# Kernel optimization log

Hardware: AMD Instinct MI355X
Metric: run time of the kernel (lower is better)

Reference implementation:

```python
import jax, jax.numpy as jnp
import numpy as np

NUM_HEADS = 16

def setup_inputs() -> dict:
    key = jax.random.key(0)
    k1, k2, k3 = jax.random.split(key, 3)
    B, T, C = 4, 2048, 2048
    x = jax.random.normal(k1, (B, T, C), dtype=jnp.float32)
    Wqkv = jax.random.normal(k2, (C, 3 * C), dtype=jnp.float32) * (C ** -0.5)
    bqkv = jnp.zeros((3 * C,), dtype=jnp.float32)
    Wproj = jax.random.normal(k3, (C, C), dtype=jnp.float32) * (C ** -0.5)
    bproj = jnp.zeros((C,), dtype=jnp.float32)
    return {"x": x, "Wqkv": Wqkv, "bqkv": bqkv, "Wproj": Wproj, "bproj": bproj}

def reference(x, Wqkv, bqkv, Wproj, bproj):
    B, T, C = x.shape
    H = NUM_HEADS
    D = C // H  # head_dim
    qkv = x @ Wqkv + bqkv                      # [B,T,3C]
    q, k, v = jnp.split(qkv, 3, axis=-1)
    # [B,T,C] -> [B,H,T,D]
    q = q.reshape(B, T, H, D).transpose(0, 2, 1, 3)
    k = k.reshape(B, T, H, D).transpose(0, 2, 1, 3)
    v = v.reshape(B, T, H, D).transpose(0, 2, 1, 3)
    scale = D ** -0.5
    scores = jnp.einsum('bhqd,bhkd->bhqk', q, k) * scale  # [B,H,T,T]
    causal = jnp.tril(jnp.ones((T, T), dtype=bool))
    scores = jnp.where(causal, scores, jnp.finfo(scores.dtype).min)
    attn = jax.nn.softmax(scores, axis=-1)
    out = jnp.einsum('bhqk,bhkd->bhqd', attn, v)           # [B,H,T,D]
    out = out.transpose(0, 2, 1, 3).reshape(B, T, C)
    return out @ Wproj + bproj
```

## Files before the change

kernel.cpp:

```cpp
#include <hip/hip_runtime.h>
#include <hip/hip_bf16.h>
#include <stdint.h>

typedef __attribute__((ext_vector_type(8))) short short8;
typedef __attribute__((ext_vector_type(4))) float f32x4;
typedef __attribute__((ext_vector_type(16))) float f32x16;
typedef __attribute__((ext_vector_type(2))) unsigned int uint2v;

__device__ __forceinline__ unsigned short f2bf(float f) {
  union { float f; unsigned int u; } v; v.f = f;
  unsigned int r = v.u + 0x7FFFu + ((v.u >> 16) & 1u);
  return (unsigned short)(r >> 16);
}

__device__ __forceinline__ unsigned int cvtpk(float lo, float hi) {
  unsigned int r;
  asm("v_cvt_pk_bf16_f32 %0, %1, %2" : "=v"(r) : "v"(lo), "v"(hi));
  return r;
}

#define GLOAD16(gsrc, ldst)                                                                  \
  __builtin_amdgcn_global_load_lds((const __attribute__((address_space(1))) void*)(gsrc),    \
                                   (__attribute__((address_space(3))) void*)(ldst), 16, 0, 0)

#define BAR() __builtin_amdgcn_s_barrier()
#define LGKMC(n) do { asm volatile("s_waitcnt lgkmcnt(" #n ")" ::: "memory"); \
                      __builtin_amdgcn_sched_barrier(0); } while (0)
#define LGKM0() LGKMC(0)
#define VMCNT0() asm volatile("s_waitcnt vmcnt(0)" ::: "memory")
#define VMCNT8() do { asm volatile("s_waitcnt vmcnt(8)" ::: "memory"); \
                      __builtin_amdgcn_sched_barrier(0); } while (0)
#define PRIO(x) __builtin_amdgcn_s_setprio(x)
#define MFMA16(d, a, b) d = __builtin_amdgcn_mfma_f32_16x16x32_bf16(a, b, d, 0, 0, 0)

__global__ __launch_bounds__(256) void preproc_kernel(const float* __restrict__ x,
                                                      const float* __restrict__ Wqkv,
                                                      const float* __restrict__ Wproj,
                                                      unsigned short* __restrict__ x_bf,
                                                      unsigned short* __restrict__ wqkvt,
                                                      unsigned short* __restrict__ wprojt) {
  __shared__ float tile[32][33];
  int blk = blockIdx.x;
  int tid = threadIdx.x;
  if (blk < 16384) {
    int i = blk * 256 + tid;
    float4 v = ((const float4*)x)[i];
    ushort4 o;
    o.x = f2bf(v.x); o.y = f2bf(v.y); o.z = f2bf(v.z); o.w = f2bf(v.w);
    ((ushort4*)x_bf)[i] = o;
    return;
  }
  const float* W;
  unsigned short* Wt;
  int n0, k0, N;
  if (blk < 16384 + 12288) {
    int b = blk - 16384;
    W = Wqkv; Wt = wqkvt; N = 6144;
    n0 = (b % 192) * 32; k0 = (b / 192) * 32;
  } else {
    int b = blk - 16384 - 12288;
    W = Wproj; Wt = wprojt; N = 2048;
    n0 = (b & 63) * 32; k0 = (b >> 6) * 32;
  }
  int tx = tid & 31, ty = tid >> 5;
#pragma unroll
  for (int j = 0; j < 32; j += 8)
    tile[ty + j][tx] = W[(size_t)(k0 + ty + j) * N + n0 + tx];
  __syncthreads();
#pragma unroll
  for (int j = 0; j < 32; j += 8)
    Wt[(size_t)(n0 + ty + j) * 2048 + k0 + tx] = f2bf(tile[tx][ty + j]);
}

__device__ __forceinline__ void stageA128(const unsigned short* __restrict__ gp, int K,
                                          int kt, char* lds, int tid) {
#pragma unroll
  for (int it = 0; it < 4; ++it) {
    int li = it * 256 + tid;
    int r = li >> 3, c = li & 7;
    GLOAD16(gp + (size_t)r * K + kt * 64 + (c ^ (r & 7)) * 8, lds + li * 16);
  }
}
__device__ __forceinline__ void stageB256(const unsigned short* __restrict__ gp, int K,
                                          int kt, char* lds, int tid) {
#pragma unroll
  for (int it = 0; it < 8; ++it) {
    int li = it * 256 + tid;
    int r = li >> 3, c = li & 7;
    GLOAD16(gp + (size_t)r * K + kt * 64 + (c ^ (r & 7)) * 8, lds + li * 16);
  }
}

__device__ __forceinline__ void gemm128x256_mainloop(const unsigned short* __restrict__ Ap,
                                                     const unsigned short* __restrict__ Bp,
                                                     int K, int tid, char* smem,
                                                     f32x4 acc[4][8]) {
  char* sa = smem;
  char* sb = smem + 16384;
  const int KT = K >> 6;

  int wid = tid >> 6, lane = tid & 63;
  int wr = wid >> 1, wc = wid & 1;
  int lg = lane >> 4, l15 = lane & 15;
  int swz7 = l15 & 7;

#define LDA(m, kc) \
  (*(const short8*)((const unsigned short*)sa + (size_t)((wr * 64 + (m) * 16 + l15) * 64 + ((((kc) * 4 + lg) ^ swz7) * 8))))
#define LDB(n, kc) \
  (*(const short8*)((const unsigned short*)sb + (size_t)((wc * 128 + (n) * 16 + l15) * 64 + ((((kc) * 4 + lg) ^ swz7) * 8))))

  stageA128(Ap, K, 0, sa, tid);
  stageB256(Bp, K, 0, sb, tid);
  VMCNT0();
  BAR();

  for (int t = 0; t < KT; ++t) {
    short8 aq[4][2], bq[4][2];
#pragma unroll
    for (int m = 0; m < 4; ++m) { aq[m][0] = LDA(m, 0); aq[m][1] = LDA(m, 1); }
#pragma unroll
    for (int n = 0; n < 4; ++n) { bq[n][0] = LDB(n, 0); bq[n][1] = LDB(n, 1); }
    LGKM0();
    PRIO(1);
#pragma unroll
    for (int kc = 0; kc < 2; ++kc)
#pragma unroll
      for (int m = 0; m < 4; ++m)
#pragma unroll
        for (int n = 0; n < 4; ++n)
          MFMA16(acc[m][n], aq[m][kc], bq[n][kc]);
    PRIO(0);
#pragma unroll
    for (int n = 0; n < 4; ++n) { bq[n][0] = LDB(n + 4, 0); bq[n][1] = LDB(n + 4, 1); }
    LGKM0();
    PRIO(1);
#pragma unroll
    for (int kc = 0; kc < 2; ++kc)
#pragma unroll
      for (int m = 0; m < 4; ++m)
#pragma unroll
        for (int n = 0; n < 4; ++n)
          MFMA16(acc[m][n + 4], aq[m][kc], bq[n][kc]);
    PRIO(0);
    BAR();
    if (t + 1 < KT) {
      stageA128(Ap, K, t + 1, sa, tid);
      stageB256(Bp, K, t + 1, sb, tid);
      VMCNT0();
    }
    BAR();
  }
#undef LDA
#undef LDB
}

__device__ __forceinline__ void stage_half(const unsigned short* __restrict__ gp, int K,
                                           int kt, int half, char* lds_mat, int tid) {
#pragma unroll
  for (int it = 0; it < 2; ++it) {
    int li = half * 1024 + it * 512 + tid;
    int r = li >> 3, c = li & 7;
    int cs = c ^ (r & 7);
    GLOAD16(gp + (size_t)r * K + kt * 64 + cs * 8, lds_mat + li * 16);
  }
}

__device__ __forceinline__ void gemm256sq_mainloop(const unsigned short* __restrict__ Ap,
                                                   const unsigned short* __restrict__ Bp,
                                                   int K, int tid, char* smem,
                                                   f32x4 acc[8][4]) {
  char* sa = smem;
  char* sb = smem + 65536;
  const int KT = K >> 6;

  int wid = tid >> 6, lane = tid & 63;
  int wr = wid >> 2, wc = wid & 3;
  int lg = lane >> 4, l15 = lane & 15;
  int swz7 = l15 & 7;

#define LDA2(ab, m, kc) \
  (*(const short8*)((const unsigned short*)(ab) + (size_t)((wr * 128 + (m) * 16 + l15) * 64 + ((((kc) * 4 + lg) ^ swz7) * 8))))
#define LDB2(bb, n, kc) \
  (*(const short8*)((const unsigned short*)(bb) + (size_t)((wc * 64 + (n) * 16 + l15) * 64 + ((((kc) * 4 + lg) ^ swz7) * 8))))

  stage_half(Bp, K, 0, 0, sb, tid);
  stage_half(Bp, K, 0, 1, sb, tid);
  stage_half(Ap, K, 0, 0, sa, tid);
  stage_half(Ap, K, 0, 1, sa, tid);
  stage_half(Bp, K, 1, 0, sb + 32768, tid);
  stage_half(Bp, K, 1, 1, sb + 32768, tid);
  stage_half(Ap, K, 1, 0, sa + 32768, tid);
  stage_half(Ap, K, 1, 1, sa + 32768, tid);
  VMCNT8();
  BAR();

  for (int t = 0; t < KT; ++t) {
    int p = t & 1;
    const char* ab = sa + p * 32768;
    const char* bb = sb + p * 32768;
    int kt2 = (t + 2 < KT) ? t + 2 : KT - 1;

    short8 bq01[2][2], bq23[2][2], aq[4][2], aq2[4][2];
#pragma unroll
    for (int n = 0; n < 2; ++n) { bq01[n][0] = LDB2(bb, n, 0); bq01[n][1] = LDB2(bb, n, 1); }
#pragma unroll
    for (int m = 0; m < 4; ++m) { aq[m][0] = LDA2(ab, m, 0); aq[m][1] = LDA2(ab, m, 1); }
#pragma unroll
    for (int n = 0; n < 2; ++n) { bq23[n][0] = LDB2(bb, n + 2, 0); bq23[n][1] = LDB2(bb, n + 2, 1); }
#pragma unroll
    for (int m = 0; m < 4; ++m) { aq2[m][0] = LDA2(ab, m + 4, 0); aq2[m][1] = LDA2(ab, m + 4, 1); }

    LGKMC(12);
    PRIO(1);
#pragma unroll
    for (int kc = 0; kc < 2; ++kc)
#pragma unroll
      for (int m = 0; m < 4; ++m)
#pragma unroll
        for (int n = 0; n < 2; ++n)
          MFMA16(acc[m][n], aq[m][kc], bq01[n][kc]);
    PRIO(0);

    LGKMC(8);
    BAR();
    stage_half(Bp, K, kt2, 0, sb + p * 32768, tid);
    stage_half(Bp, K, kt2, 1, sb + p * 32768, tid);

    PRIO(1);
#pragma unroll
    for (int kc = 0; kc < 2; ++kc)
#pragma unroll
      for (int m = 0; m < 4; ++m)
#pragma unroll
        for (int n = 0; n < 2; ++n)
          MFMA16(acc[m][n + 2], aq[m][kc], bq23[n][kc]);
    PRIO(0);

    LGKMC(0);
    PRIO(1);
#pragma unroll
    for (int kc = 0; kc < 2; ++kc)
#pragma unroll
      for (int m = 0; m < 4; ++m)
#pragma unroll
        for (int n = 0; n < 2; ++n)
          MFMA16(acc[m + 4][n + 2], aq2[m][kc], bq23[n][kc]);
    PRIO(0);

    BAR();
    stage_half(Ap, K, kt2, 0, sa + p * 32768, tid);
    stage_half(Ap, K, kt2, 1, sa + p * 32768, tid);
    PRIO(1);
#pragma unroll
    for (int kc = 0; kc < 2; ++kc)
#pragma unroll
      for (int m = 0; m < 4; ++m)
#pragma unroll
        for (int n = 0; n < 2; ++n)
          MFMA16(acc[m + 4][n], aq2[m][kc], bq01[n][kc]);
    PRIO(0);
    VMCNT8();
    BAR();
  }
#undef LDA2
#undef LDB2
}

__global__ __launch_bounds__(256, 2) void gemm_qkv256_kernel(const unsigned short* __restrict__ A,
                                                             const unsigned short* __restrict__ Bt,
                                                             const float* __restrict__ bias,
                                                             unsigned short* __restrict__ qb,
                                                             unsigned short* __restrict__ kb,
                                                             unsigned short* __restrict__ vtb) {
  extern __shared__ char smem[];
  int wg = blockIdx.x;
  int xcd = wg & 7, idx = wg >> 3;
  int bn = xcd * 3 + idx % 3;
  int bm = idx / 3;
  int tid = threadIdx.x;

  f32x4 acc[4][8];
  f32x4 zero = {0.f, 0.f, 0.f, 0.f};
#pragma unroll
  for (int m = 0; m < 4; ++m)
#pragma unroll
    for (int n = 0; n < 8; ++n) acc[m][n] = zero;

  gemm128x256_mainloop(A + (size_t)bm * 128 * 2048, Bt + (size_t)bn * 256 * 2048, 2048, tid, smem, acc);

  const float QSCALE = (float)(0.08838834764831845 * 1.4426950408889634);
  int wid = tid >> 6, lane = tid & 63;
  int wr = wid >> 1, wc = wid & 1, lg = lane >> 4, l15 = lane & 15;

  if (bn >= 16) {
    int h0v = (bn - 16) * 2;
#pragma unroll
    for (int n = 0; n < 8; ++n) {
      int cl = wc * 128 + n * 16 + l15;
      float bv = bias[bn * 256 + cl];
#pragma unroll
      for (int m = 0; m < 4; ++m) {
        int rl = wr * 64 + m * 16 + lg * 4;
        unsigned int w0 = cvtpk(acc[m][n][0] + bv, acc[m][n][1] + bv);
        unsigned int w1 = cvtpk(acc[m][n][2] + bv, acc[m][n][3] + bv);
        uint2v pk = {w0, w1};
        *(uint2v*)(smem + cl * 256 + ((rl * 2) ^ ((cl & 7) << 4))) = pk;
      }
    }
    LGKM0();
    BAR();
    int b = (bm * 128) >> 11, t0 = (bm * 128) & 2047;
#pragma unroll
    for (int i = 0; i < 16; ++i) {
      int id = i * 256 + tid;
      int dloc = id >> 4, c = id & 15;
      short8 v = *(const short8*)(smem + dloc * 256 + ((c * 16) ^ ((dloc & 7) << 4)));
      int bh_ = b * 16 + h0v + (dloc >> 7);
      int d = dloc & 127;
      *(short8*)(vtb + ((size_t)bh_ * 128 + d) * 2048 + t0 + c * 8) = v;
    }
  } else {
    bool isq = (bn < 8);
#pragma unroll
    for (int n = 0; n < 8; ++n) {
      int cl = wc * 128 + n * 16 + l15;
      float bv = bias[bn * 256 + cl];
#pragma unroll
      for (int m = 0; m < 4; ++m) {
#pragma unroll
        for (int g = 0; g < 4; ++g) {
          int rl = wr * 64 + m * 16 + lg * 4 + g;
          float r = acc[m][n][g] + bv;
          if (isq) r *= QSCALE;
          *(unsigned short*)(smem + rl * 512 + ((cl * 2) ^ ((rl & 15) << 4))) = f2bf(r);
        }
      }
    }
    LGKM0();
    BAR();
    unsigned short* dst = isq ? qb : kb;
    int h0 = (bn & 7) * 2;
#pragma unroll
    for (int i = 0; i < 16; ++i) {
      int id = i * 256 + tid;
      int rl = id >> 5, c8 = id & 31;
      short8 v = *(const short8*)(smem + rl * 512 + ((c8 * 16) ^ ((rl & 15) << 4)));
      int row = bm * 128 + rl;
      int b = row >> 11, t = row & 2047;
      int h = h0 + (c8 >> 4);
      int d0 = (c8 & 15) * 8;
      *(short8*)(dst + ((size_t)(b * 16 + h) * 2048 + t) * 128 + d0) = v;
    }
  }
}

__global__ __launch_bounds__(512, 2) void gemm_proj256_kernel(const unsigned short* __restrict__ A,
                                                              const unsigned short* __restrict__ Bt,
                                                              const float* __restrict__ bias,
                                                              float* __restrict__ out) {
  extern __shared__ char smem[];
  int wg = blockIdx.x;
  int bm = wg >> 3, bn = wg & 7;
  int tid = threadIdx.x;

  f32x4 acc[8][4];
  f32x4 zero = {0.f, 0.f, 0.f, 0.f};
#pragma unroll
  for (int m = 0; m < 8; ++m)
#pragma unroll
    for (int n = 0; n < 4; ++n) acc[m][n] = zero;

  gemm256sq_mainloop(A + (size_t)bm * 256 * 2048, Bt + (size_t)bn * 256 * 2048, 2048, tid, smem, acc);

  int wid = tid >> 6, lane = tid & 63;
  int wr = wid >> 2, wc = wid & 3, lg = lane >> 4, l15 = lane & 15;
#pragma unroll
  for (int n = 0; n < 4; ++n) {
    int col = bn * 256 + wc * 64 + n * 16 + l15;
    float bv = bias[col];
#pragma unroll
    for (int m = 0; m < 8; ++m) {
#pragma unroll
      for (int g = 0; g < 4; ++g) {
        int row = bm * 256 + wr * 128 + m * 16 + lg * 4 + g;
        out[(size_t)row * 2048 + col] = acc[m][n][g] + bv;
      }
    }
  }
}

__global__ __launch_bounds__(512) void attn_kernel(const unsigned short* __restrict__ qb,
                                                   const unsigned short* __restrict__ kb,
                                                   const unsigned short* __restrict__ vtb,
                                                   unsigned short* __restrict__ ob) {
  extern __shared__ char asmem[];
  int bh = blockIdx.x;
  int pairi = blockIdx.y;
  int b = bh >> 4, h = bh & 15;
  int tid = threadIdx.x, wid = tid >> 6, lane = tid & 63;
  int l31 = lane & 31, hi = lane >> 5;

  const unsigned short* Q  = qb  + (size_t)bh * 2048 * 128;
  const unsigned short* K  = kb  + (size_t)bh * 2048 * 128;
  const unsigned short* Vt = vtb + (size_t)bh * 128 * 2048;

#pragma unroll 1
  for (int pass = 0; pass < 2; ++pass) {
    int qt = pass == 0 ? (7 - pairi) : pairi;
    int NT = 4 * qt + 4;
    int qbase = qt * 256 + wid * 32;
    int qrow = qbase + l31;

    short8 qf[8];
#pragma unroll
    for (int kc = 0; kc < 8; ++kc)
      qf[kc] = *(const short8*)(Q + (size_t)qrow * 128 + kc * 16 + hi * 8);

    f32x16 o0 = {}, o1 = {}, o2 = {}, o3 = {};
    float m_run = -1e30f, l_run = 0.f;

    {
      char* kb_ = asmem;
#pragma unroll
      for (int it = 0; it < 2; ++it) {
        int li = it * 512 + tid;
        int r = li >> 4, c = li & 15;
        GLOAD16(K + (size_t)r * 128 + (c ^ (r & 7)) * 8, kb_ + li * 16);
      }
#pragma unroll
      for (int it = 0; it < 2; ++it) {
        int li = it * 512 + tid;
        int r = li >> 3, c = li & 7;
        GLOAD16(Vt + (size_t)r * 2048 + (c ^ (r & 7)) * 8, kb_ + 16384 + li * 16);
      }
    }
    VMCNT0();
    BAR();

#pragma unroll 1
    for (int kt = 0; kt < NT; ++kt) {
      char* cb = asmem + ((kt & 1) << 15);
      if (kt + 1 < NT) {
        char* nb = asmem + (((kt + 1) & 1) << 15);
        int kt1 = kt + 1;
#pragma unroll
        for (int it = 0; it < 2; ++it) {
          int li = it * 512 + tid;
          int r = li >> 4, c = li & 15;
          GLOAD16(K + (size_t)(kt1 * 64 + r) * 128 + (c ^ (r & 7)) * 8, nb + li * 16);
        }
#pragma unroll
        for (int it = 0; it < 2; ++it) {
          int li = it * 512 + tid;
          int r = li >> 3, c = li & 7;
          GLOAD16(Vt + (size_t)r * 2048 + kt1 * 64 + (c ^ (r & 7)) * 8, nb + 16384 + li * 16);
        }
      }

      bool active = (kt * 64 <= qbase + 31);
      if (active) {
        const char* k_l = cb;
        const char* v_l = cb + 16384;

        f32x16 s0v = {}, s1v = {};
        PRIO(1);
#pragma unroll
        for (int kc = 0; kc < 8; ++kc) {
          int cg = kc * 2 + hi;
          int sw = l31 & 7;
          short8 kf0 = *(const short8*)(k_l + l31 * 256 + ((cg ^ sw) * 16));
          s0v = __builtin_amdgcn_mfma_f32_32x32x16_bf16(kf0, qf[kc], s0v, 0, 0, 0);
          short8 kf1 = *(const short8*)(k_l + (32 + l31) * 256 + ((cg ^ sw) * 16));
          s1v = __builtin_amdgcn_mfma_f32_32x32x16_bf16(kf1, qf[kc], s1v, 0, 0, 0);
        }
        PRIO(0);

        if (kt * 64 + 63 > qbase) {
          int kvb = kt * 64 + 4 * hi;
#pragma unroll
          for (int r = 0; r < 16; ++r) {
            int kv = kvb + (r & 3) + 8 * (r >> 2);
            if (kv > qrow) s0v[r] = -1e30f;
            if (kv + 32 > qrow) s1v[r] = -1e30f;
          }
        }

        float tmax[16];
#pragma unroll
        for (int i = 0; i < 16; ++i) tmax[i] = fmaxf(s0v[i], s1v[i]);
#pragma unroll
        for (int st = 8; st >= 1; st >>= 1)
#pragma unroll
          for (int i = 0; i < st; ++i) tmax[i] = fmaxf(tmax[i], tmax[i + st]);
        float pmax = fmaxf(tmax[0], __shfl_xor(tmax[0], 32));

        if (!__all(pmax <= m_run + 8.0f)) {
          float mn = fmaxf(m_run, pmax);
          float alpha = exp2f(m_run - mn);
          m_run = mn; l_run *= alpha;
          o0 *= alpha; o1 *= alpha; o2 *= alpha; o3 *= alpha;
        }

#pragma unroll
        for (int i = 0; i < 16; ++i) {
          s0v[i] = exp2f(s0v[i] - m_run);
          s1v[i] = exp2f(s1v[i] - m_run);
        }
        float tsum[16];
#pragma unroll
        for (int i = 0; i < 16; ++i) tsum[i] = s0v[i] + s1v[i];
#pragma unroll
        for (int st = 8; st >= 1; st >>= 1)
#pragma unroll
          for (int i = 0; i < st; ++i) tsum[i] += tsum[i + st];
        float rsum = tsum[0] + __shfl_xor(tsum[0], 32);
        l_run += rsum;

#define BUILD_PA(sv, base, out)                                                \
        {                                                                      \
          unsigned int a_ = cvtpk(sv[base + 0], sv[base + 1]);                 \
          unsigned int c_ = cvtpk(sv[base + 2], sv[base + 3]);                 \
          unsigned int b_ = cvtpk(sv[base + 4], sv[base + 5]);                 \
          unsigned int d_ = cvtpk(sv[base + 6], sv[base + 7]);                 \
          uint2v r0_ = __builtin_amdgcn_permlane32_swap(a_, b_, false, false); \
          uint2v r1_ = __builtin_amdgcn_permlane32_swap(c_, d_, false, false); \
          union { unsigned int u[4]; short8 v; } uu_;                          \
          uu_.u[0] = r0_[0]; uu_.u[1] = r1_[0]; uu_.u[2] = r0_[1]; uu_.u[3] = r1_[1]; \
          out = uu_.v;                                                         \
        }
        short8 pa0, pa1, pa2, pa3;
        BUILD_PA(s0v, 0, pa0);
        BUILD_PA(s0v, 8, pa1);
        BUILD_PA(s1v, 0, pa2);
        BUILD_PA(s1v, 8, pa3);
#undef BUILD_PA

        PRIO(1);
#define PV_STEP(ovar, dt)                                                          \
        {                                                                          \
          int rv_ = dt * 32 + l31;                                                 \
          const char* vb_ = v_l + rv_ * 128;                                       \
          int sw_ = rv_ & 7;                                                       \
          short8 v0_ = *(const short8*)(vb_ + (((0 + hi) ^ sw_) * 16));            \
          ovar = __builtin_amdgcn_mfma_f32_32x32x16_bf16(v0_, pa0, ovar, 0, 0, 0); \
          short8 v1_ = *(const short8*)(vb_ + (((2 + hi) ^ sw_) * 16));            \
          ovar = __builtin_amdgcn_mfma_f32_32x32x16_bf16(v1_, pa1, ovar, 0, 0, 0); \
          short8 v2_ = *(const short8*)(vb_ + (((4 + hi) ^ sw_) * 16));            \
          ovar = __builtin_amdgcn_mfma_f32_32x32x16_bf16(v2_, pa2, ovar, 0, 0, 0); \
          short8 v3_ = *(const short8*)(vb_ + (((6 + hi) ^ sw_) * 16));            \
          ovar = __builtin_amdgcn_mfma_f32_32x32x16_bf16(v3_, pa3, ovar, 0, 0, 0); \
        }
        PV_STEP(o0, 0)
        PV_STEP(o1, 1)
        PV_STEP(o2, 2)
        PV_STEP(o3, 3)
#undef PV_STEP
        PRIO(0);
      }

      VMCNT0();
      BAR();
    }

    float inv = 1.0f / l_run;
    size_t orow = (size_t)(b * 2048 + qt * 256 + wid * 32 + l31);
    unsigned short* ob_p = ob + orow * 2048 + h * 128;
#define STORE_DT(ovar, dt)                                                         \
    {                                                                              \
      _Pragma("unroll")                                                            \
      for (int rq = 0; rq < 4; ++rq) {                                             \
        unsigned int w0 = cvtpk(ovar[rq * 4 + 0] * inv, ovar[rq * 4 + 1] * inv);   \
        unsigned int w1 = cvtpk(ovar[rq * 4 + 2] * inv, ovar[rq * 4 + 3] * inv);   \
        uint2v st = {w0, w1};                                                      \
        *(uint2v*)(ob_p + dt * 32 + rq * 8 + 4 * hi) = st;                         \
      }                                                                            \
    }
    STORE_DT(o0, 0)
    STORE_DT(o1, 1)
    STORE_DT(o2, 2)
    STORE_DT(o3, 3)
#undef STORE_DT
  }
}

extern "C" void kernel_launch(void* const* d_in, const int* in_sizes, int n_in,
                              void* d_out, int out_size, void* d_ws, size_t ws_size,
                              hipStream_t stream) {
  const float* x     = (const float*)d_in[0];
  const float* Wqkv  = (const float*)d_in[1];
  const float* bqkv  = (const float*)d_in[2];
  const float* Wproj = (const float*)d_in[3];
  const float* bproj = (const float*)d_in[4];
  float* out = (float*)d_out;

  char* ws = (char*)d_ws;
  unsigned short* x_bf   = (unsigned short*)ws;
  unsigned short* wqkvt  = (unsigned short*)(ws + 33554432);
  unsigned short* wprojt = (unsigned short*)(ws + 33554432 + 25165824);
  unsigned short* qb     = (unsigned short*)(ws + 67108864);
  unsigned short* kb     = (unsigned short*)(ws + 100663296);
  unsigned short* vtb    = (unsigned short*)(ws + 134217728);

  (void)hipFuncSetAttribute((const void*)gemm_qkv256_kernel,
                            hipFuncAttributeMaxDynamicSharedMemorySize, 65536);
  (void)hipFuncSetAttribute((const void*)gemm_proj256_kernel,
                            hipFuncAttributeMaxDynamicSharedMemorySize, 131072);
  (void)hipFuncSetAttribute((const void*)attn_kernel,
                            hipFuncAttributeMaxDynamicSharedMemorySize, 65536);

  preproc_kernel<<<32768, 256, 0, stream>>>(x, Wqkv, Wproj, x_bf, wqkvt, wprojt);
  gemm_qkv256_kernel<<<1536, 256, 65536, stream>>>(x_bf, wqkvt, bqkv, qb, kb, vtb);
  attn_kernel<<<dim3(64, 4), 512, 65536, stream>>>(qb, kb, vtb, x_bf );
  gemm_proj256_kernel<<<256, 512, 131072, stream>>>(x_bf, wprojt, bproj, out);
}
```

Baseline: 390.6 us.

## Load QKV GEMM A operand directly from global into registers with prefetch

The 128x256 QKV GEMM mainloop no longer stages the A tile through LDS. Each wave now loads its A fragments straight from global memory into registers, one k-tile ahead, double-buffered by unrolling the loop by two. Only the B tile still goes through LDS. This removes LDS traffic and the staging bandwidth for A and overlaps A loads with MFMA work. In exchange it adds register pressure and uncoalesced-ish 16-byte global reads that rely on cache hits, and the VMCNT0 wait for B also blocks on the prefetched A loads.

```diff
diff --git a/kernel.cpp b/kernel.cpp
--- a/kernel.cpp
+++ b/kernel.cpp
@@ -72,15 +72,6 @@
     Wt[(size_t)(n0 + ty + j) * 2048 + k0 + tx] = f2bf(tile[tx][ty + j]);
 }
 
-__device__ __forceinline__ void stageA128(const unsigned short* __restrict__ gp, int K,
-                                          int kt, char* lds, int tid) {
-#pragma unroll
-  for (int it = 0; it < 4; ++it) {
-    int li = it * 256 + tid;
-    int r = li >> 3, c = li & 7;
-    GLOAD16(gp + (size_t)r * K + kt * 64 + (c ^ (r & 7)) * 8, lds + li * 16);
-  }
-}
 __device__ __forceinline__ void stageB256(const unsigned short* __restrict__ gp, int K,
                                           int kt, char* lds, int tid) {
 #pragma unroll
@@ -91,66 +82,74 @@
   }
 }
 
-__device__ __forceinline__ void gemm128x256_mainloop(const unsigned short* __restrict__ Ap,
-                                                     const unsigned short* __restrict__ Bp,
-                                                     int K, int tid, char* smem,
-                                                     f32x4 acc[4][8]) {
-  char* sa = smem;
-  char* sb = smem + 16384;
+__device__ __forceinline__ void gemm128x256r_mainloop(const unsigned short* __restrict__ Ap,
+                                                      const unsigned short* __restrict__ Bp,
+                                                      int K, int tid, char* smem,
+                                                      f32x4 acc[4][8]) {
+  char* sb = smem;
   const int KT = K >> 6;
 
   int wid = tid >> 6, lane = tid & 63;
   int wr = wid >> 1, wc = wid & 1;
   int lg = lane >> 4, l15 = lane & 15;
   int swz7 = l15 & 7;
-
-#define LDA(m, kc) \
-  (*(const short8*)((const unsigned short*)sa + (size_t)((wr * 64 + (m) * 16 + l15) * 64 + ((((kc) * 4 + lg) ^ swz7) * 8))))
+  const unsigned short* abase = Ap + (size_t)(wr * 64 + l15) * K + lg * 8;
+
+#define AG(m, kc, t) (*(const short8*)(abase + (size_t)(m) * 16 * K + (t) * 64 + (kc) * 32))
 #define LDB(n, kc) \
   (*(const short8*)((const unsigned short*)sb + (size_t)((wc * 128 + (n) * 16 + l15) * 64 + ((((kc) * 4 + lg) ^ swz7) * 8))))
 
-  stageA128(Ap, K, 0, sa, tid);
+  short8 aqA[4][2], aqB[4][2];
+#pragma unroll
+  for (int m = 0; m < 4; ++m) { aqA[m][0] = AG(m, 0, 0); aqA[m][1] = AG(m, 1, 0); }
   stageB256(Bp, K, 0, sb, tid);
   VMCNT0();
   BAR();
 
-  for (int t = 0; t < KT; ++t) {
-    short8 aq[4][2], bq[4][2];
-#pragma unroll
-    for (int m = 0; m < 4; ++m) { aq[m][0] = LDA(m, 0); aq[m][1] = LDA(m, 1); }
-#pragma unroll
-    for (int n = 0; n < 4; ++n) { bq[n][0] = LDB(n, 0); bq[n][1] = LDB(n, 1); }
-    LGKM0();
-    PRIO(1);
-#pragma unroll
-    for (int kc = 0; kc < 2; ++kc)
-#pragma unroll
-      for (int m = 0; m < 4; ++m)
-#pragma unroll
-        for (int n = 0; n < 4; ++n)
-          MFMA16(acc[m][n], aq[m][kc], bq[n][kc]);
-    PRIO(0);
-#pragma unroll
-    for (int n = 0; n < 4; ++n) { bq[n][0] = LDB(n + 4, 0); bq[n][1] = LDB(n + 4, 1); }
-    LGKM0();
-    PRIO(1);
-#pragma unroll
-    for (int kc = 0; kc < 2; ++kc)
-#pragma unroll
-      for (int m = 0; m < 4; ++m)
-#pragma unroll
-        for (int n = 0; n < 4; ++n)
-          MFMA16(acc[m][n + 4], aq[m][kc], bq[n][kc]);
-    PRIO(0);
-    BAR();
-    if (t + 1 < KT) {
-      stageA128(Ap, K, t + 1, sa, tid);
-      stageB256(Bp, K, t + 1, sb, tid);
-      VMCNT0();
-    }
-    BAR();
-  }
-#undef LDA
+#define TILE_BODY(tcur, AQ, AQN)                                                       \
+  {                                                                                    \
+    int tn_ = ((tcur) + 1 < KT) ? (tcur) + 1 : KT - 1;                                 \
+    _Pragma("unroll")                                                                  \
+    for (int m = 0; m < 4; ++m) { AQN[m][0] = AG(m, 0, tn_); AQN[m][1] = AG(m, 1, tn_); } \
+    short8 bq[4][2];                                                                   \
+    _Pragma("unroll")                                                                  \
+    for (int n = 0; n < 4; ++n) { bq[n][0] = LDB(n, 0); bq[n][1] = LDB(n, 1); }        \
+    LGKM0();                                                                           \
+    PRIO(1);                                                                           \
+    _Pragma("unroll")                                                                  \
+    for (int kc = 0; kc < 2; ++kc)                                                     \
+      _Pragma("unroll")                                                                \
+      for (int m = 0; m < 4; ++m)                                                      \
+        _Pragma("unroll")                                                              \
+        for (int n = 0; n < 4; ++n)                                                    \
+          MFMA16(acc[m][n], AQ[m][kc], bq[n][kc]);                                     \
+    PRIO(0);                                                                           \
+    _Pragma("unroll")                                                                  \
+    for (int n = 0; n < 4; ++n) { bq[n][0] = LDB(n + 4, 0); bq[n][1] = LDB(n + 4, 1); } \
+    LGKM0();                                                                           \
+    PRIO(1);                                                                           \
+    _Pragma("unroll")                                                                  \
+    for (int kc = 0; kc < 2; ++kc)                                                     \
+      _Pragma("unroll")                                                                \
+      for (int m = 0; m < 4; ++m)                                                      \
+        _Pragma("unroll")                                                              \
+        for (int n = 0; n < 4; ++n)                                                    \
+          MFMA16(acc[m][n + 4], AQ[m][kc], bq[n][kc]);                                 \
+    PRIO(0);                                                                           \
+    BAR();                                                                             \
+    if ((tcur) + 1 < KT) {                                                             \
+      stageB256(Bp, K, (tcur) + 1, sb, tid);                                           \
+      VMCNT0();                                                                        \
+    }                                                                                  \
+    BAR();                                                                             \
+  }
+
+  for (int tt = 0; tt < KT; tt += 2) {
+    TILE_BODY(tt, aqA, aqB)
+    TILE_BODY(tt + 1, aqB, aqA)
+  }
+#undef TILE_BODY
+#undef AG
 #undef LDB
 }
 
@@ -286,7 +285,7 @@
 #pragma unroll
     for (int n = 0; n < 8; ++n) acc[m][n] = zero;
 
-  gemm128x256_mainloop(A + (size_t)bm * 128 * 2048, Bt + (size_t)bn * 256 * 2048, 2048, tid, smem, acc);
+  gemm128x256r_mainloop(A + (size_t)bm * 128 * 2048, Bt + (size_t)bn * 256 * 2048, 2048, tid, smem, acc);
 
   const float QSCALE = (float)(0.08838834764831845 * 1.4426950408889634);
   int wid = tid >> 6, lane = tid & 63;
```

New measurement: 527.4 us. +35.0%, slower.
